# Performance work log

Hardware: AMD Instinct MI355X
Metric: run time of the kernel (lower is better)

The kernel has to match this reference:

```python
import jax, jax.numpy as jnp
from jax import lax
import numpy as np

NC = 3              # immutable color channels
HIDDEN = 16         # hidden state channels
STATE = NC + HIDDEN # 19
PV = 5              # perception vectors per channel
PERC = PV * STATE   # 95
MID = 128


def setup_inputs() -> dict:
    key = jax.random.key(0)
    ks = jax.random.split(key, 7)
    x = jax.random.uniform(ks[0], (4, NC, 128, 128), dtype=jnp.float32)
    # grouped 3x3 conv: groups=STATE, 1 in-ch -> PV out-ch per group; OIHW kernel (95,1,3,3)
    Wp = jax.random.normal(ks[1], (PERC, 1, 3, 3), dtype=jnp.float32) * 0.1
    bp = jax.random.normal(ks[2], (PERC,), dtype=jnp.float32) * 0.01
    W1 = jax.random.normal(ks[3], (MID, PERC), dtype=jnp.float32) * 0.05
    b1 = jax.random.normal(ks[4], (MID,), dtype=jnp.float32) * 0.01
    W2 = jax.random.normal(ks[5], (HIDDEN, MID), dtype=jnp.float32) * 0.05
    b2 = jax.random.normal(ks[6], (HIDDEN,), dtype=jnp.float32) * 0.01
    return {"x": x, "Wp": Wp, "bp": bp, "W1": W1, "b1": b1, "W2": W2, "b2": b2, "steps": 16}


def _maxpool3x3(x):
    # 3x3 stride-1 pad-1 max pool over NCHW spatial dims
    return lax.reduce_window(x, -jnp.inf, lax.max,
                             (1, 1, 3, 3), (1, 1, 1, 1),
                             ((0, 0), (0, 0), (1, 1), (1, 1)))


def reference(x, Wp, bp, W1, b1, W2, b2, steps):
    N, _, H, W = x.shape
    state0 = jnp.concatenate([x, jnp.zeros((N, HIDDEN, H, W), x.dtype)], axis=1)

    def step(state, _):
        # depthwise/grouped 3x3 perception conv (groups = STATE)
        p = lax.conv_general_dilated(state, Wp, (1, 1), ((1, 1), (1, 1)),
                                     feature_group_count=STATE,
                                     dimension_numbers=("NCHW", "OIHW", "NCHW"))
        p = p + bp[None, :, None, None]
        # 1x1 conv -> LeakyReLU(0.2) -> 1x1 conv
        h = jnp.einsum("nchw,oc->nohw", p, W1) + b1[None, :, None, None]
        h = jnp.where(h >= 0, h, 0.2 * h)
        upd = jnp.einsum("nchw,oc->nohw", h, W2) + b2[None, :, None, None]
        # stochastic_update with p=1: mask = rand < 1 is always True -> plain add
        s = state.at[:, NC:].add(upd)
        # alive mask: maxpool of channel 4 > 0 gates all mutable channels
        alive = (_maxpool3x3(s[:, 4:5]) > 0).astype(s.dtype)
        s = s.at[:, NC:].multiply(alive)
        # sigmoid slice-assign on channel 4
        s = s.at[:, 4].set(jax.nn.sigmoid(s[:, 4]))
        return s, None

    final, _ = lax.scan(step, state0, None, length=steps)
    return final
```

## Files before the change

kernel.cpp:

```cpp
#include <hip/hip_runtime.h>
#include <math.h>

#define NN    4
#define NC    3
#define HID   16
#define CST   19
#define PV    5
#define PERC  95
#define MIDC  128
#define HH    128
#define WW    128
#define HW    (HH*WW)
#define STEPS 16
#define TPX   256
#define NTHR  1024
#define KP    104
#define HT    136
#define W1F_N 24576
#define W2F_N 4096

typedef short  bf16x8 __attribute__((ext_vector_type(8)));
typedef short  bf16x4 __attribute__((ext_vector_type(4)));
typedef float  f32x4v __attribute__((ext_vector_type(4)));

__device__ __forceinline__ unsigned short f2bf_rtn(float f) {
    unsigned u = __float_as_uint(f);
    u += 0x7FFFu + ((u >> 16) & 1u);
    return (unsigned short)(u >> 16);
}
__device__ __forceinline__ float bf2f(unsigned short h) {
    return __uint_as_float(((unsigned)h) << 16);
}
__device__ __forceinline__ void bfsplit(float a, short& hi, short& lo) {
    unsigned short hb = f2bf_rtn(a);
    hi = (short)hb;
    lo = (short)f2bf_rtn(a - bf2f(hb));
}

__global__ __launch_bounds__(1024) void nca_wprep(
        short* __restrict__ wf,
        const float* __restrict__ W1, const float* __restrict__ W2) {
    const int tid = threadIdx.x;
    for (int e = tid; e < W1F_N; e += 1024) {
        int j = e & 7, lane = (e >> 3) & 63, q = e >> 9;
        int ch = q % 12, wrow = q / 12;
        int hl = ch & 1, t = ch >> 1, ks = t % 3, mt = t / 3;
        int lw = lane & 15, g = lane >> 4;
        int m  = wrow * 32 + mt * 16 + lw;
        int kk = ks * 32 + g * 8 + j;
        float av = (kk < PERC) ? W1[m * PERC + kk] : 0.0f;
        short hi, lo; bfsplit(av, hi, lo);
        wf[e] = hl ? lo : hi;
    }
    for (int e = tid; e < W2F_N; e += 1024) {
        int j = e & 7, lane = (e >> 3) & 63, q = e >> 9;
        int hl = q & 1, ks = q >> 1;
        int lw = lane & 15, g = lane >> 4;
        float av = W2[lw * MIDC + ks * 32 + g * 8 + j];
        short hi, lo; bfsplit(av, hi, lo);
        wf[W1F_N + e] = hl ? lo : hi;
    }
}

__global__ __launch_bounds__(NTHR) void nca_fused(
        const float* __restrict__ tmp_in,  long istride,
        float* __restrict__ tmp_out,       long ostride,
        const float* __restrict__ x,
        const short* __restrict__ wscr,
        const float* __restrict__ Wp, const float* __restrict__ bp,
        const float* __restrict__ b1, const float* __restrict__ b2,
        int first) {
    const int n       = blockIdx.x >> 6;
    const int pixbase = (blockIdx.x & 63) * TPX;
    const int y0      = pixbase >> 7;
    const int tid     = threadIdx.x;
    const int lane    = tid & 63;
    const int w       = __builtin_amdgcn_readfirstlane(tid >> 6);
    const int wrow    = w >> 2;
    const int wcol    = w & 3;
    const int lw      = lane & 15;
    const int g       = lane >> 4;
    const int g8      = g * 8;

    __shared__ __align__(16) unsigned char raw[139840];
    short* p_hi  = (short*)raw;
    short* p_lo  = p_hi + 256 * KP;
    short* h_hi  = (short*)raw;
    short* h_lo  = (short*)(raw + 69632);
    float* stile = (float*)(raw + 106496);
    float* b1tab = (float*)(raw + 139264);
    float* b2tab = (float*)(raw + 139776);

    if (tid < MIDC) b1tab[tid] = b1[tid];
    else if (tid < MIDC + HID) b2tab[tid - MIDC] = b2[tid - MIDC];

    {
        const int u2   = tid & 511;
        const int half = tid >> 9;
        const int px   = u2 & 127;
        const int yy   = y0 - 1 + (u2 >> 7);
        if (!first && yy >= 0 && yy < HH) {
            const float* tb = tmp_in + (size_t)n * istride;
            const float* c1 = tb + 1 * HW;
            const int idx = (yy << 7) + px;
            const bool ym = (yy > 0), yp = (yy < HH - 1);
            const bool xm = (px > 0), xp = (px < WW - 1);
            float mx = c1[idx];
            if (ym)       mx = fmaxf(mx, c1[idx - WW]);
            if (yp)       mx = fmaxf(mx, c1[idx + WW]);
            if (xm)       mx = fmaxf(mx, c1[idx - 1]);
            if (xp)       mx = fmaxf(mx, c1[idx + 1]);
            if (ym && xm) mx = fmaxf(mx, c1[idx - WW - 1]);
            if (ym && xp) mx = fmaxf(mx, c1[idx - WW + 1]);
            if (yp && xm) mx = fmaxf(mx, c1[idx + WW - 1]);
            if (yp && xp) mx = fmaxf(mx, c1[idx + WW + 1]);
            const float alive = (mx > 0.0f) ? 1.0f : 0.0f;
#pragma unroll
            for (int cc = 0; cc < 8; ++cc) {
                const int c = half * 8 + cc;
                float v = tb[c * HW + idx] * alive;
                if (c == 1) v = 1.0f / (1.0f + expf(-v));
                stile[c * 512 + u2] = v;
            }
        } else {
#pragma unroll
            for (int cc = 0; cc < 8; ++cc)
                stile[(half * 8 + cc) * 512 + u2] = 0.0f;
        }
    }

    bf16x8 ah[2][3], al[2][3];
#pragma unroll
    for (int mt = 0; mt < 2; ++mt)
#pragma unroll
        for (int ks = 0; ks < 3; ++ks) {
            const int base = ((wrow * 12 + ((mt * 3 + ks) << 1)) * 64 + lane) * 8;
            ah[mt][ks] = *(const bf16x8*)&wscr[base];
            al[mt][ks] = *(const bf16x8*)&wscr[base + 512];
        }
    __syncthreads();

    auto conv_site = [&](int u) {
        int c = u >> 8;
        int p = u & 255;
        int y = y0 + (p >> 7);
        int xc = p & 127;
        const bool xm = (xc > 0), xp = (xc < WW - 1);
        float t00, t01, t02, t10, t11, t12, t20, t21, t22;
        if (c < NC) {
            const int gpix = (y << 7) + xc;
            const float* ch = x + ((size_t)n * NC + c) * HW;
            const bool ym = (y > 0), yp = (y < HH - 1);
            t00 = (ym && xm) ? ch[gpix - WW - 1] : 0.0f;
            t01 = ym         ? ch[gpix - WW]     : 0.0f;
            t02 = (ym && xp) ? ch[gpix - WW + 1] : 0.0f;
            t10 = xm         ? ch[gpix - 1]      : 0.0f;
            t11 =              ch[gpix];
            t12 = xp         ? ch[gpix + 1]      : 0.0f;
            t20 = (yp && xm) ? ch[gpix + WW - 1] : 0.0f;
            t21 = yp         ? ch[gpix + WW]     : 0.0f;
            t22 = (yp && xp) ? ch[gpix + WW + 1] : 0.0f;
        } else {
            const float* sr = stile + (c - NC) * 512;
            const int b = ((p >> 7) + 1) * 128 + xc;
            t00 = xm ? sr[b - 128 - 1] : 0.0f;
            t01 =      sr[b - 128];
            t02 = xp ? sr[b - 128 + 1] : 0.0f;
            t10 = xm ? sr[b - 1]       : 0.0f;
            t11 =      sr[b];
            t12 = xp ? sr[b + 1]       : 0.0f;
            t20 = xm ? sr[b + 128 - 1] : 0.0f;
            t21 =      sr[b + 128];
            t22 = xp ? sr[b + 128 + 1] : 0.0f;
        }
#pragma unroll
        for (int v = 0; v < PV; ++v) {
            const float* wv = Wp + (c * PV + v) * 9;
            float a = bp[c * PV + v];
            a += wv[0] * t00; a += wv[1] * t01; a += wv[2] * t02;
            a += wv[3] * t10; a += wv[4] * t11; a += wv[5] * t12;
            a += wv[6] * t20; a += wv[7] * t21; a += wv[8] * t22;
            const int kidx = c * PV + v;
            short h_, l_;
            bfsplit(a, h_, l_);
            p_hi[p * KP + kidx] = h_;
            p_lo[p * KP + kidx] = l_;
        }
    };
#pragma unroll
    for (int it = 0; it < 4; ++it) conv_site(it * NTHR + tid);
    if (tid < 768) conv_site(4 * NTHR + tid);
    if (tid < 256) { p_hi[tid * KP + 95] = 0; p_lo[tid * KP + 95] = 0; }
    __syncthreads();

    f32x4v acc[2][4];
#pragma unroll
    for (int mt = 0; mt < 2; ++mt)
#pragma unroll
        for (int nt = 0; nt < 4; ++nt)
            acc[mt][nt] = (f32x4v){0.0f, 0.0f, 0.0f, 0.0f};

    const int pxb = wcol * 64;
#pragma unroll
    for (int nt = 0; nt < 4; ++nt) {
#pragma unroll
        for (int ks = 0; ks < 3; ++ks) {
            const short* bp_ = &p_hi[(pxb + nt * 16 + lw) * KP + ks * 32 + g8];
            bf16x8 bh = *(const bf16x8*)bp_;
            bf16x8 bl = *(const bf16x8*)(bp_ + 256 * KP);
            acc[0][nt] = __builtin_amdgcn_mfma_f32_16x16x32_bf16(ah[0][ks], bh, acc[0][nt], 0, 0, 0);
            acc[1][nt] = __builtin_amdgcn_mfma_f32_16x16x32_bf16(ah[1][ks], bh, acc[1][nt], 0, 0, 0);
            acc[0][nt] = __builtin_amdgcn_mfma_f32_16x16x32_bf16(ah[0][ks], bl, acc[0][nt], 0, 0, 0);
            acc[1][nt] = __builtin_amdgcn_mfma_f32_16x16x32_bf16(ah[1][ks], bl, acc[1][nt], 0, 0, 0);
            acc[0][nt] = __builtin_amdgcn_mfma_f32_16x16x32_bf16(al[0][ks], bh, acc[0][nt], 0, 0, 0);
            acc[1][nt] = __builtin_amdgcn_mfma_f32_16x16x32_bf16(al[1][ks], bh, acc[1][nt], 0, 0, 0);
            acc[0][nt] = __builtin_amdgcn_mfma_f32_16x16x32_bf16(al[0][ks], bl, acc[0][nt], 0, 0, 0);
            acc[1][nt] = __builtin_amdgcn_mfma_f32_16x16x32_bf16(al[1][ks], bl, acc[1][nt], 0, 0, 0);
        }
    }

#pragma unroll
    for (int mt = 0; mt < 2; ++mt) {
        f32x4v bq = *(const f32x4v*)&b1tab[wrow * 32 + mt * 16 + g * 4];
#pragma unroll
        for (int nt = 0; nt < 4; ++nt)
#pragma unroll
            for (int r = 0; r < 4; ++r) {
                float v = acc[mt][nt][r] + bq[r];
                acc[mt][nt][r] = (v >= 0.0f) ? v : 0.2f * v;
            }
    }

    float resid[4];
    {
        const int pxe = w * 16 + lw;
#pragma unroll
        for (int r = 0; r < 4; ++r)
            resid[r] = stile[(g * 4 + r) * 512 + (1 + (pxe >> 7)) * 128 + (pxe & 127)];
    }
    __syncthreads();

#pragma unroll
    for (int mt = 0; mt < 2; ++mt)
#pragma unroll
        for (int nt = 0; nt < 4; ++nt) {
            const int px = pxb + nt * 16 + lw;
            bf16x4 hv, lv;
#pragma unroll
            for (int r = 0; r < 4; ++r) {
                unsigned short hb = f2bf_rtn(acc[mt][nt][r]);
                hv[r] = (short)hb;
                lv[r] = (short)f2bf_rtn(acc[mt][nt][r] - bf2f(hb));
            }
            const int off = px * HT + wrow * 32 + mt * 16 + g * 4;
            *(bf16x4*)&h_hi[off] = hv;
            *(bf16x4*)&h_lo[off] = lv;
        }
    bf16x8 wh[4], wl[4];
    {
        const short* w2f = wscr + W1F_N;
#pragma unroll
        for (int ks = 0; ks < 4; ++ks) {
            const int base = ((ks * 2) * 64 + lane) * 8;
            wh[ks] = *(const bf16x8*)&w2f[base];
            wl[ks] = *(const bf16x8*)&w2f[base + 512];
        }
    }
    __syncthreads();

    f32x4v acc2 = (f32x4v){0.0f, 0.0f, 0.0f, 0.0f};
#pragma unroll
    for (int ks = 0; ks < 4; ++ks) {
        const int off = (w * 16 + lw) * HT + ks * 32 + g8;
        bf16x8 bh = *(const bf16x8*)&h_hi[off];
        bf16x8 bl = *(const bf16x8*)&h_lo[off];
        acc2 = __builtin_amdgcn_mfma_f32_16x16x32_bf16(wh[ks], bh, acc2, 0, 0, 0);
        acc2 = __builtin_amdgcn_mfma_f32_16x16x32_bf16(wl[ks], bh, acc2, 0, 0, 0);
        acc2 = __builtin_amdgcn_mfma_f32_16x16x32_bf16(wh[ks], bl, acc2, 0, 0, 0);
        acc2 = __builtin_amdgcn_mfma_f32_16x16x32_bf16(wl[ks], bl, acc2, 0, 0, 0);
    }

    {
        const int px = w * 16 + lw;
        const int gp = pixbase + px;
        float* tb = tmp_out + (size_t)n * ostride;
#pragma unroll
        for (int r = 0; r < 4; ++r) {
            const int o = g * 4 + r;
            tb[(size_t)o * HW + gp] = acc2[r] + b2tab[o] + resid[r];
        }
    }
}

__global__ __launch_bounds__(256) void nca_step2(
        float* __restrict__ state,
        const float* __restrict__ tmp,
        const float* __restrict__ x) {
    int gid = blockIdx.x * 256 + threadIdx.x;
    int xx = gid & (WW - 1);
    int y = (gid >> 7) & (HH - 1);
    int n = gid >> 14;
    const int idx = y * WW + xx;

    const float* c4 = tmp + (size_t)n * HID * HW + 1 * HW;
    const bool ym = (y > 0), yp = (y < HH - 1);
    const bool xm = (xx > 0), xp = (xx < WW - 1);

    float mx = c4[idx];
    if (ym)       mx = fmaxf(mx, c4[idx - WW]);
    if (yp)       mx = fmaxf(mx, c4[idx + WW]);
    if (xm)       mx = fmaxf(mx, c4[idx - 1]);
    if (xp)       mx = fmaxf(mx, c4[idx + 1]);
    if (ym && xm) mx = fmaxf(mx, c4[idx - WW - 1]);
    if (ym && xp) mx = fmaxf(mx, c4[idx - WW + 1]);
    if (yp && xm) mx = fmaxf(mx, c4[idx + WW - 1]);
    if (yp && xp) mx = fmaxf(mx, c4[idx + WW + 1]);

    float alive = (mx > 0.0f) ? 1.0f : 0.0f;

    float* sb = state + (size_t)n * CST * HW + NC * HW + idx;
    const float* tb = tmp + (size_t)n * HID * HW + idx;
#pragma unroll
    for (int i = 0; i < HID; ++i) {
        float v = tb[i * HW] * alive;
        if (i == 1) v = 1.0f / (1.0f + expf(-v));
        sb[i * HW] = v;
    }
    float* cb = state + (size_t)n * CST * HW + idx;
#pragma unroll
    for (int c = 0; c < NC; ++c)
        cb[(size_t)c * HW] = x[((size_t)n * NC + c) * HW + idx];
}

extern "C" void kernel_launch(void* const* d_in, const int* in_sizes, int n_in,
                              void* d_out, int out_size, void* d_ws, size_t ws_size,
                              hipStream_t stream) {
    const float* x  = (const float*)d_in[0];
    const float* Wp = (const float*)d_in[1];
    const float* bp = (const float*)d_in[2];
    const float* W1 = (const float*)d_in[3];
    const float* b1 = (const float*)d_in[4];
    const float* W2 = (const float*)d_in[5];
    const float* b2 = (const float*)d_in[6];

    float* state = (float*)d_out;
    float* ws    = (float*)d_ws;

    short* wscr = (short*)state;

    float* bufA = state + (size_t)NC * HW;
    const long strideA = (long)CST * HW;
    float* bufB = ws;
    const long strideB = (long)HID * HW;

    nca_wprep<<<1, 1024, 0, stream>>>(wscr, W1, W2);

    const int blocks1 = (NN * HW) / TPX;
    for (int s = 0; s < STEPS; ++s) {
        const float* tin;  long sin;
        float*       tout; long sout;
        if ((s & 1) == 0) { tin = bufB; sin = strideB; tout = bufA; sout = strideA; }
        else              { tin = bufA; sin = strideA; tout = bufB; sout = strideB; }
        nca_fused<<<blocks1, NTHR, 0, stream>>>(tin, sin, tout, sout,
                                                x, wscr, Wp, bp, b1, b2,
                                                (s == 0) ? 1 : 0);
    }
    nca_step2<<<(NN * HW) / 256, 256, 0, stream>>>(state, ws, x);
}
```

Measured before the change: 352.1 us.

## Interleave bf16 hi/lo splits in LDS, overlap x-channel conv, remap block tiles

Hi and lo bf16 halves of the perception and hidden activations are now packed into one 32-bit word and stored interleaved in shared memory. Each fragment load becomes two 128-bit reads followed by register unpacking, replacing two separate plane reads, and the split values are written with single stores. The conv stage is split so the immutable-channel sites, which read global x, run before the barrier that publishes the hidden-state tile, overlapping those global loads with tile setup. The block-to-tile mapping is also permuted, which changes the order in which tiles are scheduled across CUs. The unpacking adds VALU work, and the interleaved layout may change LDS bank-conflict behaviour.

After: 324.5 us. -7.8%, faster.

```diff
diff --git a/kernel.cpp b/kernel.cpp
--- a/kernel.cpp
+++ b/kernel.cpp
@@ -20,7 +20,6 @@
 #define W2F_N 4096
 
 typedef short  bf16x8 __attribute__((ext_vector_type(8)));
-typedef short  bf16x4 __attribute__((ext_vector_type(4)));
 typedef float  f32x4v __attribute__((ext_vector_type(4)));
 
 __device__ __forceinline__ unsigned short f2bf_rtn(float f) {
@@ -35,6 +34,11 @@
     unsigned short hb = f2bf_rtn(a);
     hi = (short)hb;
     lo = (short)f2bf_rtn(a - bf2f(hb));
+}
+__device__ __forceinline__ unsigned packsplit(float a) {
+    unsigned short hb = f2bf_rtn(a);
+    unsigned short lb = f2bf_rtn(a - bf2f(hb));
+    return ((unsigned)hb << 16) | (unsigned)lb;
 }
 
 __global__ __launch_bounds__(1024) void nca_wprep(
@@ -70,8 +74,9 @@
         const float* __restrict__ Wp, const float* __restrict__ bp,
         const float* __restrict__ b1, const float* __restrict__ b2,
         int first) {
-    const int n       = blockIdx.x >> 6;
-    const int pixbase = (blockIdx.x & 63) * TPX;
+    const int tile    = ((blockIdx.x & 7) << 5) + (blockIdx.x >> 3);
+    const int n       = tile >> 6;
+    const int pixbase = (tile & 63) * TPX;
     const int y0      = pixbase >> 7;
     const int tid     = threadIdx.x;
     const int lane    = tid & 63;
@@ -83,13 +88,11 @@
     const int g8      = g * 8;
 
     __shared__ __align__(16) unsigned char raw[139840];
-    short* p_hi  = (short*)raw;
-    short* p_lo  = p_hi + 256 * KP;
-    short* h_hi  = (short*)raw;
-    short* h_lo  = (short*)(raw + 69632);
-    float* stile = (float*)(raw + 106496);
-    float* b1tab = (float*)(raw + 139264);
-    float* b2tab = (float*)(raw + 139776);
+    unsigned* pp    = (unsigned*)raw;
+    unsigned* hp    = (unsigned*)raw;
+    float*    stile = (float*)(raw + 106496);
+    float*    b1tab = (float*)(raw + 139264);
+    float*    b2tab = (float*)(raw + 139776);
 
     if (tid < MIDC) b1tab[tid] = b1[tid];
     else if (tid < MIDC + HID) b2tab[tid - MIDC] = b2[tid - MIDC];
@@ -138,41 +141,10 @@
             ah[mt][ks] = *(const bf16x8*)&wscr[base];
             al[mt][ks] = *(const bf16x8*)&wscr[base + 512];
         }
-    __syncthreads();
-
-    auto conv_site = [&](int u) {
-        int c = u >> 8;
-        int p = u & 255;
-        int y = y0 + (p >> 7);
-        int xc = p & 127;
-        const bool xm = (xc > 0), xp = (xc < WW - 1);
-        float t00, t01, t02, t10, t11, t12, t20, t21, t22;
-        if (c < NC) {
-            const int gpix = (y << 7) + xc;
-            const float* ch = x + ((size_t)n * NC + c) * HW;
-            const bool ym = (y > 0), yp = (y < HH - 1);
-            t00 = (ym && xm) ? ch[gpix - WW - 1] : 0.0f;
-            t01 = ym         ? ch[gpix - WW]     : 0.0f;
-            t02 = (ym && xp) ? ch[gpix - WW + 1] : 0.0f;
-            t10 = xm         ? ch[gpix - 1]      : 0.0f;
-            t11 =              ch[gpix];
-            t12 = xp         ? ch[gpix + 1]      : 0.0f;
-            t20 = (yp && xm) ? ch[gpix + WW - 1] : 0.0f;
-            t21 = yp         ? ch[gpix + WW]     : 0.0f;
-            t22 = (yp && xp) ? ch[gpix + WW + 1] : 0.0f;
-        } else {
-            const float* sr = stile + (c - NC) * 512;
-            const int b = ((p >> 7) + 1) * 128 + xc;
-            t00 = xm ? sr[b - 128 - 1] : 0.0f;
-            t01 =      sr[b - 128];
-            t02 = xp ? sr[b - 128 + 1] : 0.0f;
-            t10 = xm ? sr[b - 1]       : 0.0f;
-            t11 =      sr[b];
-            t12 = xp ? sr[b + 1]       : 0.0f;
-            t20 = xm ? sr[b + 128 - 1] : 0.0f;
-            t21 =      sr[b + 128];
-            t22 = xp ? sr[b + 128 + 1] : 0.0f;
-        }
+
+    auto conv_emit = [&](int c, int p, float t00, float t01, float t02,
+                         float t10, float t11, float t12,
+                         float t20, float t21, float t22) {
 #pragma unroll
         for (int v = 0; v < PV; ++v) {
             const float* wv = Wp + (c * PV + v) * 9;
@@ -180,17 +152,53 @@
             a += wv[0] * t00; a += wv[1] * t01; a += wv[2] * t02;
             a += wv[3] * t10; a += wv[4] * t11; a += wv[5] * t12;
             a += wv[6] * t20; a += wv[7] * t21; a += wv[8] * t22;
-            const int kidx = c * PV + v;
-            short h_, l_;
-            bfsplit(a, h_, l_);
-            p_hi[p * KP + kidx] = h_;
-            p_lo[p * KP + kidx] = l_;
+            pp[p * KP + c * PV + v] = packsplit(a);
         }
     };
-#pragma unroll
-    for (int it = 0; it < 4; ++it) conv_site(it * NTHR + tid);
-    if (tid < 768) conv_site(4 * NTHR + tid);
-    if (tid < 256) { p_hi[tid * KP + 95] = 0; p_lo[tid * KP + 95] = 0; }
+
+    if (tid < 768) {
+        const int c = tid >> 8;
+        const int p = tid & 255;
+        const int y = y0 + (p >> 7);
+        const int xc = p & 127;
+        const bool xm = (xc > 0), xp = (xc < WW - 1);
+        const int gpix = (y << 7) + xc;
+        const float* ch = x + ((size_t)n * NC + c) * HW;
+        const bool ym = (y > 0), yp = (y < HH - 1);
+        float t00 = (ym && xm) ? ch[gpix - WW - 1] : 0.0f;
+        float t01 = ym         ? ch[gpix - WW]     : 0.0f;
+        float t02 = (ym && xp) ? ch[gpix - WW + 1] : 0.0f;
+        float t10 = xm         ? ch[gpix - 1]      : 0.0f;
+        float t11 =              ch[gpix];
+        float t12 = xp         ? ch[gpix + 1]      : 0.0f;
+        float t20 = (yp && xm) ? ch[gpix + WW - 1] : 0.0f;
+        float t21 = yp         ? ch[gpix + WW]     : 0.0f;
+        float t22 = (yp && xp) ? ch[gpix + WW + 1] : 0.0f;
+        conv_emit(c, p, t00, t01, t02, t10, t11, t12, t20, t21, t22);
+    }
+    if (tid < 256) pp[tid * KP + 95] = 0;
+    __syncthreads();
+
+#pragma unroll
+    for (int it = 0; it < 4; ++it) {
+        const int u = 768 + it * NTHR + tid;
+        const int c = u >> 8;
+        const int p = u & 255;
+        const int xc = p & 127;
+        const bool xm = (xc > 0), xp = (xc < WW - 1);
+        const float* sr = stile + (c - NC) * 512;
+        const int b = ((p >> 7) + 1) * 128 + xc;
+        float t00 = xm ? sr[b - 128 - 1] : 0.0f;
+        float t01 =      sr[b - 128];
+        float t02 = xp ? sr[b - 128 + 1] : 0.0f;
+        float t10 = xm ? sr[b - 1]       : 0.0f;
+        float t11 =      sr[b];
+        float t12 = xp ? sr[b + 1]       : 0.0f;
+        float t20 = xm ? sr[b + 128 - 1] : 0.0f;
+        float t21 =      sr[b + 128];
+        float t22 = xp ? sr[b + 128 + 1] : 0.0f;
+        conv_emit(c, p, t00, t01, t02, t10, t11, t12, t20, t21, t22);
+    }
     __syncthreads();
 
     f32x4v acc[2][4];
@@ -205,9 +213,17 @@
     for (int nt = 0; nt < 4; ++nt) {
 #pragma unroll
         for (int ks = 0; ks < 3; ++ks) {
-            const short* bp_ = &p_hi[(pxb + nt * 16 + lw) * KP + ks * 32 + g8];
-            bf16x8 bh = *(const bf16x8*)bp_;
-            bf16x8 bl = *(const bf16x8*)(bp_ + 256 * KP);
+            const unsigned* pq = &pp[(pxb + nt * 16 + lw) * KP + ks * 32 + g8];
+            uint4 qa = *(const uint4*)pq;
+            uint4 qb = *(const uint4*)(pq + 4);
+            const unsigned q[8] = {qa.x, qa.y, qa.z, qa.w,
+                                   qb.x, qb.y, qb.z, qb.w};
+            bf16x8 bh, bl;
+#pragma unroll
+            for (int j = 0; j < 8; ++j) {
+                bh[j] = (short)(q[j] >> 16);
+                bl[j] = (short)(q[j] & 0xffffu);
+            }
             acc[0][nt] = __builtin_amdgcn_mfma_f32_16x16x32_bf16(ah[0][ks], bh, acc[0][nt], 0, 0, 0);
             acc[1][nt] = __builtin_amdgcn_mfma_f32_16x16x32_bf16(ah[1][ks], bh, acc[1][nt], 0, 0, 0);
             acc[0][nt] = __builtin_amdgcn_mfma_f32_16x16x32_bf16(ah[0][ks], bl, acc[0][nt], 0, 0, 0);
@@ -245,16 +261,12 @@
 #pragma unroll
         for (int nt = 0; nt < 4; ++nt) {
             const int px = pxb + nt * 16 + lw;
-            bf16x4 hv, lv;
-#pragma unroll
-            for (int r = 0; r < 4; ++r) {
-                unsigned short hb = f2bf_rtn(acc[mt][nt][r]);
-                hv[r] = (short)hb;
-                lv[r] = (short)f2bf_rtn(acc[mt][nt][r] - bf2f(hb));
-            }
-            const int off = px * HT + wrow * 32 + mt * 16 + g * 4;
-            *(bf16x4*)&h_hi[off] = hv;
-            *(bf16x4*)&h_lo[off] = lv;
+            uint4 hv;
+            hv.x = packsplit(acc[mt][nt][0]);
+            hv.y = packsplit(acc[mt][nt][1]);
+            hv.z = packsplit(acc[mt][nt][2]);
+            hv.w = packsplit(acc[mt][nt][3]);
+            *(uint4*)&hp[px * HT + wrow * 32 + mt * 16 + g * 4] = hv;
         }
     bf16x8 wh[4], wl[4];
     {
@@ -271,9 +283,17 @@
     f32x4v acc2 = (f32x4v){0.0f, 0.0f, 0.0f, 0.0f};
 #pragma unroll
     for (int ks = 0; ks < 4; ++ks) {
-        const int off = (w * 16 + lw) * HT + ks * 32 + g8;
-        bf16x8 bh = *(const bf16x8*)&h_hi[off];
-        bf16x8 bl = *(const bf16x8*)&h_lo[off];
+        const unsigned* hq = &hp[(w * 16 + lw) * HT + ks * 32 + g8];
+        uint4 qa = *(const uint4*)hq;
+        uint4 qb = *(const uint4*)(hq + 4);
+        const unsigned q[8] = {qa.x, qa.y, qa.z, qa.w,
+                               qb.x, qb.y, qb.z, qb.w};
+        bf16x8 bh, bl;
+#pragma unroll
+        for (int j = 0; j < 8; ++j) {
+            bh[j] = (short)(q[j] >> 16);
+            bl[j] = (short)(q[j] & 0xffffu);
+        }
         acc2 = __builtin_amdgcn_mfma_f32_16x16x32_bf16(wh[ks], bh, acc2, 0, 0, 0);
         acc2 = __builtin_amdgcn_mfma_f32_16x16x32_bf16(wl[ks], bh, acc2, 0, 0, 0);
         acc2 = __builtin_amdgcn_mfma_f32_16x16x32_bf16(wh[ks], bl, acc2, 0, 0, 0);
```
